# Optimization experiments

Measured on AMD Instinct MI355X. Metric: run time of the kernel, lower is better.

Reference implementation:

```python
import jax, jax.numpy as jnp
import numpy as np

N_NODES = 10000


def gcn_conv(x, W, b, src, dst, n):
    # GCNConv (PyG defaults): linear transform, add self-loops, symmetric norm,
    # scatter-add aggregation at target nodes, then bias.
    h = x @ W  # [n, out]
    # degree with self-loops: 1 (self) + count of incoming edges per target node
    deg = jnp.ones((n,), h.dtype).at[dst].add(1.0)
    dinv = jax.lax.rsqrt(deg)  # deg >= 1 always
    norm = dinv[src] * dinv[dst]  # [E]
    # edge messages + self-loop contribution (norm_ii = dinv_i^2)
    agg = jnp.zeros_like(h).at[dst].add(h[src] * norm[:, None])
    agg = agg + h * (dinv * dinv)[:, None]
    return agg + b


def setup_inputs() -> dict:
    key = jax.random.key(0)
    ks = jax.random.split(key, 8)
    d_in, d_hid, d_out = 512, 512, 100
    n, e = N_NODES, 160000
    x = jax.random.normal(ks[0], (n, d_in), dtype=jnp.float32)
    edge_index = jax.random.randint(ks[1], (2, e), 0, n, dtype=jnp.int64)
    s1 = 1.0 / np.sqrt(d_in)
    s2 = 1.0 / np.sqrt(d_hid)
    W1 = jax.random.uniform(ks[2], (d_in, d_hid), jnp.float32, -s1, s1)
    b1 = jnp.zeros((d_hid,), jnp.float32)
    W2 = jax.random.uniform(ks[3], (d_hid, d_hid), jnp.float32, -s2, s2)
    b2 = jnp.zeros((d_hid,), jnp.float32)
    Wc = jax.random.uniform(ks[4], (d_hid, d_out), jnp.float32, -s2, s2)
    bc = jax.random.uniform(ks[5], (d_out,), jnp.float32, -s2, s2)
    return {"x": x, "edge_index": edge_index, "W1": W1, "b1": b1,
            "W2": W2, "b2": b2, "Wc": Wc, "bc": bc}


def reference(x, edge_index, W1, b1, W2, b2, Wc, bc):
    src, dst = edge_index[0], edge_index[1]
    n = x.shape[0]
    h = gcn_conv(x, W1, b1, src, dst, n)
    h = jax.nn.relu(h)  # dropout is identity in eval mode
    h = gcn_conv(h, W2, b2, src, dst, n)
    return h @ Wc + bc
```

## Files before the change

### kernel.cpp

```cpp
#include <hip/hip_runtime.h>
#include <hip/hip_bf16.h>
#include <stdint.h>

typedef __bf16 bf16_t;
typedef bf16_t bf16x8 __attribute__((ext_vector_type(8)));
typedef float f32x4 __attribute__((ext_vector_type(4)));

#define NN 10000
#define ELLCAP 64

__device__ __forceinline__ float b2f(unsigned short u) {
  union { unsigned int i; float f; } c; c.i = ((unsigned int)u) << 16; return c.f;
}
__device__ __forceinline__ unsigned short f2b(float f) {
  union { float f; unsigned int i; } c; c.f = f;
  unsigned int x = c.i;
  x += 0x7FFFu + ((x >> 16) & 1u);
  return (unsigned short)(x >> 16);
}
__device__ __forceinline__ uint4 cvt8(float4 a, float4 b) {
  uint4 r;
  r.x = (unsigned int)f2b(a.x) | ((unsigned int)f2b(a.y) << 16);
  r.y = (unsigned int)f2b(a.z) | ((unsigned int)f2b(a.w) << 16);
  r.z = (unsigned int)f2b(b.x) | ((unsigned int)f2b(b.y) << 16);
  r.w = (unsigned int)f2b(b.z) | ((unsigned int)f2b(b.w) << 16);
  return r;
}
__device__ __forceinline__ void load_lds16(const void* g, void* l) {
  __builtin_amdgcn_global_load_lds(
      (const __attribute__((address_space(1))) unsigned int*)g,
      (__attribute__((address_space(3))) unsigned int*)l, 16, 0, 0);
}
__device__ __forceinline__ f32x4 mfma16(bf16x8 a, bf16x8 b, f32x4 c) {
  return __builtin_amdgcn_mfma_f32_16x16x32_bf16(a, b, c, 0, 0, 0);
}

template <bool SCALED>
__device__ void gemm64(const unsigned short* __restrict__ A, const unsigned short* __restrict__ Bt,
                       unsigned short* __restrict__ C, const int* __restrict__ cntp,
                       int M, int Ncols, int ldc, int tm, int tn,
                       unsigned short* __restrict__ As, unsigned short* __restrict__ Bs)
{
  const int tid = threadIdx.x;
  const int lane = tid & 63;
  const int wn = tid >> 6;
  const int quad = lane >> 4, l15 = lane & 15;

  const int r0 = tid >> 2, kc = tid & 3;
  int ga = tm * 64 + r0;  if (ga > M - 1) ga = M - 1;
  const int gb0 = tn * 128 + r0;
  const int gb1 = tn * 128 + 64 + r0;
  const unsigned short* gA  = A + (size_t)ga * 512 + kc * 8;
  const unsigned short* gB0 = Bt + (size_t)gb0 * 512 + kc * 8;
  const unsigned short* gB1 = Bt + (size_t)gb1 * 512 + kc * 8;
  const int loff  = r0 * 32 + kc * 8;
  const int loff1 = (64 + r0) * 32 + kc * 8;
  const int ABUF = 64 * 32, BBUF = 128 * 32;

  f32x4 acc[4][2];
  #pragma unroll
  for (int i = 0; i < 4; i++)
    #pragma unroll
    for (int j = 0; j < 2; j++) {
      f32x4 z = {0.f, 0.f, 0.f, 0.f};
      acc[i][j] = z;
    }

  load_lds16(gA,  &As[loff]);
  load_lds16(gB0, &Bs[loff]);
  load_lds16(gB1, &Bs[loff1]);
  __syncthreads();

  for (int it = 0; it < 16; ++it) {
    const int ca = (it & 1) * ABUF, cb = (it & 1) * BBUF;
    if (it < 15) {
      const int k1 = (it + 1) * 32;
      const int na = ((it & 1) ^ 1) * ABUF, nb = ((it & 1) ^ 1) * BBUF;
      load_lds16(gA + k1,  &As[na + loff]);
      load_lds16(gB0 + k1, &Bs[nb + loff]);
      load_lds16(gB1 + k1, &Bs[nb + loff1]);
    }
    bf16x8 af[4], bfr[2];
    #pragma unroll
    for (int i = 0; i < 4; i++)
      af[i] = *(const bf16x8*)&As[ca + (i * 16 + l15) * 32 + quad * 8];
    #pragma unroll
    for (int j = 0; j < 2; j++)
      bfr[j] = *(const bf16x8*)&Bs[cb + (wn * 32 + j * 16 + l15) * 32 + quad * 8];
    #pragma unroll
    for (int i = 0; i < 4; i++)
      #pragma unroll
      for (int j = 0; j < 2; j++)
        acc[i][j] = mfma16(af[i], bfr[j], acc[i][j]);
    __syncthreads();
  }

  #pragma unroll
  for (int i = 0; i < 4; i++) {
    #pragma unroll
    for (int r = 0; r < 4; r++) {
      const int row = tm * 64 + i * 16 + quad * 4 + r;
      if (row < M) {
        float dv = 1.f;
        if (SCALED) {
          int c = cntp[row]; if (c > ELLCAP) c = ELLCAP;
          dv = rsqrtf((float)(1 + c));
        }
        #pragma unroll
        for (int j = 0; j < 2; j++) {
          const int col = tn * 128 + wn * 32 + j * 16 + l15;
          if (col < Ncols)
            C[(size_t)row * ldc + col] = f2b(acc[i][j][r] * dv);
        }
      }
    }
  }
}

__device__ void gemm64_f32A(const float* __restrict__ A, const unsigned short* __restrict__ Bt,
                            unsigned short* __restrict__ C, const int* __restrict__ cntp,
                            int M, int tm, int tn,
                            unsigned short* __restrict__ As, unsigned short* __restrict__ Bs)
{
  const int tid = threadIdx.x;
  const int lane = tid & 63;
  const int wn = tid >> 6;
  const int quad = lane >> 4, l15 = lane & 15;

  const int r0 = tid >> 2, kc = tid & 3;
  int ga = tm * 64 + r0;  if (ga > M - 1) ga = M - 1;
  const int gb0 = tn * 128 + r0;
  const int gb1 = tn * 128 + 64 + r0;
  const float* gA = A + (size_t)ga * 512 + kc * 8;
  const unsigned short* gB0 = Bt + (size_t)gb0 * 512 + kc * 8;
  const unsigned short* gB1 = Bt + (size_t)gb1 * 512 + kc * 8;
  const int loff  = r0 * 32 + kc * 8;
  const int loff1 = (64 + r0) * 32 + kc * 8;
  const int ABUF = 64 * 32, BBUF = 128 * 32;

  f32x4 acc[4][2];
  #pragma unroll
  for (int i = 0; i < 4; i++)
    #pragma unroll
    for (int j = 0; j < 2; j++) {
      f32x4 z = {0.f, 0.f, 0.f, 0.f};
      acc[i][j] = z;
    }

  {
    float4 a0 = *(const float4*)(gA), a1 = *(const float4*)(gA + 4);
    *(uint4*)&As[loff] = cvt8(a0, a1);
    load_lds16(gB0, &Bs[loff]);
    load_lds16(gB1, &Bs[loff1]);
  }
  __syncthreads();

  for (int it = 0; it < 16; ++it) {
    const int ca = (it & 1) * ABUF, cb = (it & 1) * BBUF;
    const int na = ((it & 1) ^ 1) * ABUF, nb = ((it & 1) ^ 1) * BBUF;
    float4 a0, a1;
    if (it < 15) {
      const int k1 = (it + 1) * 32;
      a0 = *(const float4*)(gA + k1);  a1 = *(const float4*)(gA + k1 + 4);
      load_lds16(gB0 + k1, &Bs[nb + loff]);
      load_lds16(gB1 + k1, &Bs[nb + loff1]);
    }
    bf16x8 af[4], bfr[2];
    #pragma unroll
    for (int i = 0; i < 4; i++)
      af[i] = *(const bf16x8*)&As[ca + (i * 16 + l15) * 32 + quad * 8];
    #pragma unroll
    for (int j = 0; j < 2; j++)
      bfr[j] = *(const bf16x8*)&Bs[cb + (wn * 32 + j * 16 + l15) * 32 + quad * 8];
    #pragma unroll
    for (int i = 0; i < 4; i++)
      #pragma unroll
      for (int j = 0; j < 2; j++)
        acc[i][j] = mfma16(af[i], bfr[j], acc[i][j]);
    if (it < 15) *(uint4*)&As[na + loff] = cvt8(a0, a1);
    __syncthreads();
  }

  #pragma unroll
  for (int i = 0; i < 4; i++) {
    #pragma unroll
    for (int r = 0; r < 4; r++) {
      const int row = tm * 64 + i * 16 + quad * 4 + r;
      if (row < M) {
        int c = cntp[row]; if (c > ELLCAP) c = ELLCAP;
        const float dv = rsqrtf((float)(1 + c));
        #pragma unroll
        for (int j = 0; j < 2; j++) {
          const int col = tn * 128 + wn * 32 + j * 16 + l15;
          C[(size_t)row * 512 + col] = f2b(acc[i][j][r] * dv);
        }
      }
    }
  }
}

__device__ void wtrans_tile(const float* __restrict__ W, unsigned short* __restrict__ Wt,
                            int ncols, int tr0, int tc0)
{
  __shared__ float tile[64][65];
  const int t = threadIdx.x;
  const int r = t >> 2, c4 = t & 3;
  #pragma unroll
  for (int i = 0; i < 4; i++) {
    int col = c4 * 16 + i * 4;
    int gc = tc0 + col;
    float4 v;
    if (gc + 3 < ncols) {
      v = *(const float4*)&W[(size_t)(tr0 + r) * ncols + gc];
    } else {
      v.x = (gc + 0 < ncols) ? W[(size_t)(tr0 + r) * ncols + gc + 0] : 0.f;
      v.y = (gc + 1 < ncols) ? W[(size_t)(tr0 + r) * ncols + gc + 1] : 0.f;
      v.z = (gc + 2 < ncols) ? W[(size_t)(tr0 + r) * ncols + gc + 2] : 0.f;
      v.w = (gc + 3 < ncols) ? W[(size_t)(tr0 + r) * ncols + gc + 3] : 0.f;
    }
    tile[r][col] = v.x; tile[r][col + 1] = v.y;
    tile[r][col + 2] = v.z; tile[r][col + 3] = v.w;
  }
  __syncthreads();
  const int o = t >> 2;
  #pragma unroll
  for (int i = 0; i < 4; i++) {
    int k = c4 * 16 + i * 4;
    ushort4 u;
    u.x = f2b(tile[k + 0][o]); u.y = f2b(tile[k + 1][o]);
    u.z = f2b(tile[k + 2][o]); u.w = f2b(tile[k + 3][o]);
    *(ushort4*)&Wt[(size_t)(tc0 + o) * 512 + tr0 + k] = u;
  }
}

__global__ __launch_bounds__(256)
void prep_fill(const float* __restrict__ W1, const float* __restrict__ Wc,
               const float* __restrict__ W2, const int* __restrict__ src,
               const int* __restrict__ dst, int* __restrict__ cnt,
               int* __restrict__ ell, unsigned short* __restrict__ W1t,
               unsigned short* __restrict__ Wct, unsigned short* __restrict__ w2b, int E)
{
  if (blockIdx.x < 64) { wtrans_tile(W1, W1t, 512, (blockIdx.x >> 3) * 64, (blockIdx.x & 7) * 64); return; }
  if (blockIdx.x < 80) { int b = blockIdx.x - 64; wtrans_tile(Wc, Wct, 100, (b >> 1) * 64, (b & 1) * 64); return; }
  const int t0 = (blockIdx.x - 80) * 256 + threadIdx.x;
  const int FT = 160 * 256;
  const float4* W24 = (const float4*)W2;
  uint4* w2b4 = (uint4*)w2b;
  for (int i = t0; i < 512 * 512 / 8; i += FT)
    w2b4[i] = cvt8(W24[i * 2], W24[i * 2 + 1]);
  for (int e = t0; e < E; e += FT) {
    int s = src[e], d = dst[e];
    int pos = atomicAdd(&cnt[d], 1);
    if (pos < ELLCAP) ell[d * ELLCAP + pos] = s;
  }
}

__global__ __launch_bounds__(256)
void gemm1_fold(const float* __restrict__ x, const unsigned short* __restrict__ W1t,
                unsigned short* __restrict__ B2, const int* __restrict__ cnt,
                const unsigned short* __restrict__ Wct, const unsigned short* __restrict__ w2b,
                unsigned short* __restrict__ W2WcT,
                const float* __restrict__ b2, const float* __restrict__ Wc,
                const float* __restrict__ bc, float* __restrict__ bias2c)
{
  __shared__ __align__(16) unsigned short As[2 * 64 * 32];
  __shared__ __align__(16) unsigned short Bs[2 * 128 * 32];
  const int b = blockIdx.x;
  if (b < 628) {
    const int xcd = b & 7, loc = b >> 3;
    const int base = (xcd < 4) ? xcd * 79 : 316 + (xcd - 4) * 78;
    const int t = base + loc;
    gemm64_f32A(x, W1t, B2, cnt, NN, t >> 2, t & 3, As, Bs);
  } else if (b < 636) {
    const int g = b - 628;
    gemm64<false>(Wct, w2b, W2WcT, nullptr, 128, 512, 512, g >> 2, g & 3, As, Bs);
  } else {
    const int j = threadIdx.x;
    if (j < 128) {
      float s = 0.f;
      if (j < 100) {
        s = bc[j];
        for (int k = 0; k < 512; k++) s = fmaf(b2[k], Wc[k * 100 + j], s);
      }
      bias2c[j] = s;
    }
  }
}

__device__ __forceinline__ void add8(float* a, uint4 v) {
  a[0] += b2f((unsigned short)(v.x & 0xffffu));
  a[1] += b2f((unsigned short)(v.x >> 16));
  a[2] += b2f((unsigned short)(v.y & 0xffffu));
  a[3] += b2f((unsigned short)(v.y >> 16));
  a[4] += b2f((unsigned short)(v.z & 0xffffu));
  a[5] += b2f((unsigned short)(v.z >> 16));
  a[6] += b2f((unsigned short)(v.w & 0xffffu));
  a[7] += b2f((unsigned short)(v.w >> 16));
}

__global__ __launch_bounds__(256)
void gather1(const unsigned short* __restrict__ h, const int* __restrict__ cnt,
             const int* __restrict__ ell, const float* __restrict__ bias,
             unsigned short* __restrict__ outb, int n)
{
  int node = blockIdx.x * 4 + (threadIdx.x >> 6);
  if (node >= n) return;
  const int lane = threadIdx.x & 63;
  const int c8 = lane * 8;

  int cd = cnt[node]; if (cd > ELLCAP) cd = ELLCAP;
  const float dinv = rsqrtf((float)(1 + cd));
  uint4 hv = *(const uint4*)&h[(size_t)node * 512 + c8];
  float a[8] = {0.f, 0.f, 0.f, 0.f, 0.f, 0.f, 0.f, 0.f};
  add8(a, hv);

  const int* row = ell + node * ELLCAP;
  int j = 0;
  for (; j + 8 <= cd; j += 8) {
    int ss[8]; uint4 vv[8];
    #pragma unroll
    for (int q = 0; q < 8; q++) ss[q] = row[j + q];
    #pragma unroll
    for (int q = 0; q < 8; q++) vv[q] = *(const uint4*)&h[(size_t)ss[q] * 512 + c8];
    #pragma unroll
    for (int q = 0; q < 8; q++) add8(a, vv[q]);
  }
  for (; j < cd; ++j) {
    int s = row[j];
    uint4 v = *(const uint4*)&h[(size_t)s * 512 + c8];
    add8(a, v);
  }

  const float4* bp = (const float4*)&bias[c8];
  float4 b0 = bp[0], b1 = bp[1];
  float bb[8] = {b0.x, b0.y, b0.z, b0.w, b1.x, b1.y, b1.z, b1.w};
  #pragma unroll
  for (int q = 0; q < 8; q++) a[q] = fmaxf(fmaf(a[q], dinv, bb[q]), 0.f);
  uint4 o;
  o.x = (unsigned int)f2b(a[0]) | ((unsigned int)f2b(a[1]) << 16);
  o.y = (unsigned int)f2b(a[2]) | ((unsigned int)f2b(a[3]) << 16);
  o.z = (unsigned int)f2b(a[4]) | ((unsigned int)f2b(a[5]) << 16);
  o.w = (unsigned int)f2b(a[6]) | ((unsigned int)f2b(a[7]) << 16);
  *(uint4*)&outb[(size_t)node * 512 + c8] = o;
}

__global__ __launch_bounds__(256)
void gemm2c(const unsigned short* __restrict__ B1, const unsigned short* __restrict__ W2WcT,
            unsigned short* __restrict__ Z, const int* __restrict__ cnt)
{
  __shared__ __align__(16) unsigned short As[2 * 64 * 32];
  __shared__ __align__(16) unsigned short Bs[2 * 128 * 32];
  gemm64<true>(B1, W2WcT, Z, cnt, NN, 128, 128, blockIdx.x, 0, As, Bs);
}

__global__ __launch_bounds__(256)
void gather2c(const unsigned short* __restrict__ Z, const int* __restrict__ cnt,
              const int* __restrict__ ell, const float* __restrict__ bias2c,
              float* __restrict__ out, int n)
{
  int node = blockIdx.x * 4 + (threadIdx.x >> 6);
  if (node >= n) return;
  const int lane = threadIdx.x & 63;
  const int c2 = lane * 2;

  int cd = cnt[node]; if (cd > ELLCAP) cd = ELLCAP;
  const float dinv = rsqrtf((float)(1 + cd));
  unsigned int hv = *(const unsigned int*)&Z[(size_t)node * 128 + c2];
  float a0 = b2f((unsigned short)(hv & 0xffffu));
  float a1 = b2f((unsigned short)(hv >> 16));

  const int* row = ell + node * ELLCAP;
  int j = 0;
  for (; j + 8 <= cd; j += 8) {
    int ss[8]; unsigned int vv[8];
    #pragma unroll
    for (int q = 0; q < 8; q++) ss[q] = row[j + q];
    #pragma unroll
    for (int q = 0; q < 8; q++) vv[q] = *(const unsigned int*)&Z[(size_t)ss[q] * 128 + c2];
    #pragma unroll
    for (int q = 0; q < 8; q++) {
      a0 += b2f((unsigned short)(vv[q] & 0xffffu));
      a1 += b2f((unsigned short)(vv[q] >> 16));
    }
  }
  for (; j < cd; ++j) {
    int s = row[j];
    unsigned int v = *(const unsigned int*)&Z[(size_t)s * 128 + c2];
    a0 += b2f((unsigned short)(v & 0xffffu));
    a1 += b2f((unsigned short)(v >> 16));
  }
  if (c2 < 100) {
    const float2 bb = *(const float2*)&bias2c[c2];
    *(float2*)&out[(size_t)node * 100 + c2] =
        make_float2(fmaf(a0, dinv, bb.x), fmaf(a1, dinv, bb.y));
  }
}

extern "C" void kernel_launch(void* const* d_in, const int* in_sizes, int n_in,
                              void* d_out, int out_size, void* d_ws, size_t ws_size,
                              hipStream_t stream) {
  const float* x  = (const float*)d_in[0];
  const int*   ei = (const int*)d_in[1];
  const float* W1 = (const float*)d_in[2];
  const float* b1 = (const float*)d_in[3];
  const float* W2 = (const float*)d_in[4];
  const float* b2 = (const float*)d_in[5];
  const float* Wc = (const float*)d_in[6];
  const float* bc = (const float*)d_in[7];
  float* out = (float*)d_out;

  const int n = NN;
  const int E = in_sizes[1] / 2;
  const int* src = ei;
  const int* dst = ei + E;

  char* w = (char*)d_ws;
  int* cnt = (int*)w;                       w += ((n * 4 + 255) / 256) * 256;
  int* ell = (int*)w;                       w += ((n * ELLCAP * 4 + 255) / 256) * 256;
  float* bias2c = (float*)w;                w += 512;
  unsigned short* W1t = (unsigned short*)w; w += 512 * 512 * 2;
  unsigned short* Wct = (unsigned short*)w; w += 128 * 512 * 2;
  unsigned short* w2b = (unsigned short*)w; w += 512 * 512 * 2;
  unsigned short* W2WcT = (unsigned short*)w; w += 128 * 512 * 2;
  unsigned short* B1  = (unsigned short*)w; w += (size_t)n * 512 * 2;
  unsigned short* B2  = (unsigned short*)w; w += (size_t)n * 512 * 2;
  unsigned short* Z   = (unsigned short*)w; w += (size_t)n * 128 * 2;

  const int nb_g = (n + 3) / 4;

  hipMemsetAsync(cnt, 0, n * sizeof(int), stream);
  prep_fill<<<240, 256, 0, stream>>>(W1, Wc, W2, src, dst, cnt, ell, W1t, Wct, w2b, E);
  gemm1_fold<<<637, 256, 0, stream>>>(x, W1t, B2, cnt, Wct, w2b, W2WcT, b2, Wc, bc, bias2c);
  gather1<<<nb_g, 256, 0, stream>>>(B2, cnt, ell, b1, B1, n);
  gemm2c<<<157, 256, 0, stream>>>(B1, W2WcT, Z, cnt);
  gather2c<<<nb_g, 256, 0, stream>>>(Z, cnt, ell, bias2c, out, n);
}
```

Before: 156.9 us.

## Overlap ELL construction with first GEMM and move source normalization into gather

The edge-to-ELL fill moves out of the prep kernel and into extra blocks of the first GEMM launch, so it runs alongside the x·W1 GEMM. The separate memset is replaced by zeroing cnt inside the prep kernel. The source-side rsqrt degree scaling is dropped from the GEMM epilogue, which no longer reads cnt. The gather instead computes a per-edge norm from each neighbour's count and folds the bias in at the start. This removes a launch and a serial phase, at the cost of an extra scattered cnt load per edge in the gather, and neighbour counts there are no longer clamped to ELLCAP.

```diff
diff --git a/kernel.cpp b/kernel.cpp
--- a/kernel.cpp
+++ b/kernel.cpp
@@ -118,8 +118,7 @@
 }
 
 __device__ void gemm64_f32A(const float* __restrict__ A, const unsigned short* __restrict__ Bt,
-                            unsigned short* __restrict__ C, const int* __restrict__ cntp,
-                            int M, int tm, int tn,
+                            unsigned short* __restrict__ C, int M, int tm, int tn,
                             unsigned short* __restrict__ As, unsigned short* __restrict__ Bs)
 {
   const int tid = threadIdx.x;
@@ -187,12 +186,10 @@
     for (int r = 0; r < 4; r++) {
       const int row = tm * 64 + i * 16 + quad * 4 + r;
       if (row < M) {
-        int c = cntp[row]; if (c > ELLCAP) c = ELLCAP;
-        const float dv = rsqrtf((float)(1 + c));
         #pragma unroll
         for (int j = 0; j < 2; j++) {
           const int col = tn * 128 + wn * 32 + j * 16 + l15;
-          C[(size_t)row * 512 + col] = f2b(acc[i][j][r] * dv);
+          C[(size_t)row * 512 + col] = f2b(acc[i][j][r]);
         }
       }
     }
@@ -234,11 +231,10 @@
 }
 
 __global__ __launch_bounds__(256)
-void prep_fill(const float* __restrict__ W1, const float* __restrict__ Wc,
-               const float* __restrict__ W2, const int* __restrict__ src,
-               const int* __restrict__ dst, int* __restrict__ cnt,
-               int* __restrict__ ell, unsigned short* __restrict__ W1t,
-               unsigned short* __restrict__ Wct, unsigned short* __restrict__ w2b, int E)
+void prep1(const float* __restrict__ W1, const float* __restrict__ Wc,
+           const float* __restrict__ W2, int* __restrict__ cnt,
+           unsigned short* __restrict__ W1t, unsigned short* __restrict__ Wct,
+           unsigned short* __restrict__ w2b)
 {
   if (blockIdx.x < 64) { wtrans_tile(W1, W1t, 512, (blockIdx.x >> 3) * 64, (blockIdx.x & 7) * 64); return; }
   if (blockIdx.x < 80) { int b = blockIdx.x - 64; wtrans_tile(Wc, Wct, 100, (b >> 1) * 64, (b & 1) * 64); return; }
@@ -248,20 +244,18 @@
   uint4* w2b4 = (uint4*)w2b;
   for (int i = t0; i < 512 * 512 / 8; i += FT)
     w2b4[i] = cvt8(W24[i * 2], W24[i * 2 + 1]);
-  for (int e = t0; e < E; e += FT) {
-    int s = src[e], d = dst[e];
-    int pos = atomicAdd(&cnt[d], 1);
-    if (pos < ELLCAP) ell[d * ELLCAP + pos] = s;
-  }
+  if (t0 < NN) cnt[t0] = 0;
 }
 
 __global__ __launch_bounds__(256)
-void gemm1_fold(const float* __restrict__ x, const unsigned short* __restrict__ W1t,
-                unsigned short* __restrict__ B2, const int* __restrict__ cnt,
-                const unsigned short* __restrict__ Wct, const unsigned short* __restrict__ w2b,
-                unsigned short* __restrict__ W2WcT,
-                const float* __restrict__ b2, const float* __restrict__ Wc,
-                const float* __restrict__ bc, float* __restrict__ bias2c)
+void gemm1_fold_ell(const float* __restrict__ x, const unsigned short* __restrict__ W1t,
+                    unsigned short* __restrict__ B2,
+                    const unsigned short* __restrict__ Wct, const unsigned short* __restrict__ w2b,
+                    unsigned short* __restrict__ W2WcT,
+                    const float* __restrict__ b2, const float* __restrict__ Wc,
+                    const float* __restrict__ bc, float* __restrict__ bias2c,
+                    const int* __restrict__ src, const int* __restrict__ dst,
+                    int* __restrict__ cnt, int* __restrict__ ell, int E)
 {
   __shared__ __align__(16) unsigned short As[2 * 64 * 32];
   __shared__ __align__(16) unsigned short Bs[2 * 128 * 32];
@@ -270,11 +264,11 @@
     const int xcd = b & 7, loc = b >> 3;
     const int base = (xcd < 4) ? xcd * 79 : 316 + (xcd - 4) * 78;
     const int t = base + loc;
-    gemm64_f32A(x, W1t, B2, cnt, NN, t >> 2, t & 3, As, Bs);
+    gemm64_f32A(x, W1t, B2, NN, t >> 2, t & 3, As, Bs);
   } else if (b < 636) {
     const int g = b - 628;
     gemm64<false>(Wct, w2b, W2WcT, nullptr, 128, 512, 512, g >> 2, g & 3, As, Bs);
-  } else {
+  } else if (b == 636) {
     const int j = threadIdx.x;
     if (j < 128) {
       float s = 0.f;
@@ -284,18 +278,26 @@
       }
       bias2c[j] = s;
     }
-  }
-}
-
-__device__ __forceinline__ void add8(float* a, uint4 v) {
-  a[0] += b2f((unsigned short)(v.x & 0xffffu));
-  a[1] += b2f((unsigned short)(v.x >> 16));
-  a[2] += b2f((unsigned short)(v.y & 0xffffu));
-  a[3] += b2f((unsigned short)(v.y >> 16));
-  a[4] += b2f((unsigned short)(v.z & 0xffffu));
-  a[5] += b2f((unsigned short)(v.z >> 16));
-  a[6] += b2f((unsigned short)(v.w & 0xffffu));
-  a[7] += b2f((unsigned short)(v.w >> 16));
+  } else {
+    const int t0 = (b - 637) * 256 + threadIdx.x;
+    const int FT = 163 * 256;
+    for (int e = t0; e < E; e += FT) {
+      int s = src[e], d = dst[e];
+      int pos = atomicAdd(&cnt[d], 1);
+      if (pos < ELLCAP) ell[d * ELLCAP + pos] = s;
+    }
+  }
+}
+
+__device__ __forceinline__ void acc8(float* a, uint4 v, float nm) {
+  a[0] = fmaf(b2f((unsigned short)(v.x & 0xffffu)), nm, a[0]);
+  a[1] = fmaf(b2f((unsigned short)(v.x >> 16)),     nm, a[1]);
+  a[2] = fmaf(b2f((unsigned short)(v.y & 0xffffu)), nm, a[2]);
+  a[3] = fmaf(b2f((unsigned short)(v.y >> 16)),     nm, a[3]);
+  a[4] = fmaf(b2f((unsigned short)(v.z & 0xffffu)), nm, a[4]);
+  a[5] = fmaf(b2f((unsigned short)(v.z >> 16)),     nm, a[5]);
+  a[6] = fmaf(b2f((unsigned short)(v.w & 0xffffu)), nm, a[6]);
+  a[7] = fmaf(b2f((unsigned short)(v.w >> 16)),     nm, a[7]);
 }
 
 __global__ __launch_bounds__(256)
@@ -309,33 +311,34 @@
   const int c8 = lane * 8;
 
   int cd = cnt[node]; if (cd > ELLCAP) cd = ELLCAP;
-  const float dinv = rsqrtf((float)(1 + cd));
+  const float fd = (float)(1 + cd);
+  const float slf = 1.0f / fd;
   uint4 hv = *(const uint4*)&h[(size_t)node * 512 + c8];
-  float a[8] = {0.f, 0.f, 0.f, 0.f, 0.f, 0.f, 0.f, 0.f};
-  add8(a, hv);
+  const float4* bp = (const float4*)&bias[c8];
+  float4 b0 = bp[0], b1 = bp[1];
+  float a[8] = {b0.x, b0.y, b0.z, b0.w, b1.x, b1.y, b1.z, b1.w};
+  acc8(a, hv, slf);
 
   const int* row = ell + node * ELLCAP;
   int j = 0;
   for (; j + 8 <= cd; j += 8) {
-    int ss[8]; uint4 vv[8];
+    int ss[8]; uint4 vv[8]; float nm[8];
     #pragma unroll
     for (int q = 0; q < 8; q++) ss[q] = row[j + q];
     #pragma unroll
     for (int q = 0; q < 8; q++) vv[q] = *(const uint4*)&h[(size_t)ss[q] * 512 + c8];
     #pragma unroll
-    for (int q = 0; q < 8; q++) add8(a, vv[q]);
+    for (int q = 0; q < 8; q++) nm[q] = rsqrtf((float)(1 + cnt[ss[q]]) * fd);
+    #pragma unroll
+    for (int q = 0; q < 8; q++) acc8(a, vv[q], nm[q]);
   }
   for (; j < cd; ++j) {
     int s = row[j];
     uint4 v = *(const uint4*)&h[(size_t)s * 512 + c8];
-    add8(a, v);
-  }
-
-  const float4* bp = (const float4*)&bias[c8];
-  float4 b0 = bp[0], b1 = bp[1];
-  float bb[8] = {b0.x, b0.y, b0.z, b0.w, b1.x, b1.y, b1.z, b1.w};
-  #pragma unroll
-  for (int q = 0; q < 8; q++) a[q] = fmaxf(fmaf(a[q], dinv, bb[q]), 0.f);
+    acc8(a, v, rsqrtf((float)(1 + cnt[s]) * fd));
+  }
+  #pragma unroll
+  for (int q = 0; q < 8; q++) a[q] = fmaxf(a[q], 0.f);
   uint4 o;
   o.x = (unsigned int)f2b(a[0]) | ((unsigned int)f2b(a[1]) << 16);
   o.y = (unsigned int)f2b(a[2]) | ((unsigned int)f2b(a[3]) << 16);
@@ -428,9 +431,9 @@
 
   const int nb_g = (n + 3) / 4;
 
-  hipMemsetAsync(cnt, 0, n * sizeof(int), stream);
-  prep_fill<<<240, 256, 0, stream>>>(W1, Wc, W2, src, dst, cnt, ell, W1t, Wct, w2b, E);
-  gemm1_fold<<<637, 256, 0, stream>>>(x, W1t, B2, cnt, Wct, w2b, W2WcT, b2, Wc, bc, bias2c);
+  prep1<<<240, 256, 0, stream>>>(W1, Wc, W2, cnt, W1t, Wct, w2b);
+  gemm1_fold_ell<<<800, 256, 0, stream>>>(x, W1t, B2, Wct, w2b, W2WcT,
+                                          b2, Wc, bc, bias2c, src, dst, cnt, ell, E);
   gather1<<<nb_g, 256, 0, stream>>>(B2, cnt, ell, b1, B1, n);
   gemm2c<<<157, 256, 0, stream>>>(B1, W2WcT, Z, cnt);
   gather2c<<<nb_g, 256, 0, stream>>>(Z, cnt, ell, bias2c, out, n);
```

Measured after the change: 151.5 us. -3.4%, faster.
